# Kernel tuning notes

Measured on AMD Instinct MI355X. Metric: run time of the kernel, lower is better.

## Reference

```python
import jax, jax.numpy as jnp
import numpy as np

E, T, H, IN = 12, 2048, 64, 128  # edge types, notes, hidden, input feat


def setup_inputs() -> dict:
    key = jax.random.key(0)
    ks = jax.random.split(key, 9)
    std_a = (2.0 / (H + H)) ** 0.5
    std_b = (2.0 / (IN + H)) ** 0.5
    std_c = (2.0 / (H * E + H)) ** 0.5
    return {
        "input": jax.random.normal(ks[0], (1, T, IN), jnp.float32),
        "hidden": jax.random.normal(ks[1], (1, T, H), jnp.float32),
        # dense per-edge-type adjacency, scaled small for stable recurrence
        "edge_matrix": jax.random.normal(ks[2], (E, T, T), jnp.float32) * 0.05,
        "ba": jnp.zeros((E, H), jnp.float32),
        "wz_wr_wh": jax.random.normal(ks[3], (E, H, 3 * H), jnp.float32) * std_c,
        "uz_ur": jax.random.normal(ks[4], (H, 2 * H), jnp.float32) * std_a,
        "uh": jax.random.normal(ks[5], (H, H), jnp.float32) * std_a,
        "input_wzrh": jax.random.normal(ks[6], (IN, 3 * H), jnp.float32) * std_b,
        "bw": jnp.zeros((3 * H,), jnp.float32),
        "iteration": 10,
    }


def reference(input, hidden, edge_matrix, ba, wz_wr_wh, uz_ur, uh, input_wzrh, bw, iteration):
    x = input[0]   # [T, IN]  (batch == 1 in this branch)
    h0 = hidden[0]  # [T, H]
    # input projection is iteration-invariant; hoist it (same math as recompute)
    iwz, iwr, iwh = jnp.split(x @ input_wzrh, 3, axis=-1)  # each [T, H]

    def step(h, _):
        # activation[e,t,h] = sum_s edge[e,s,t] * hidden[s,h]  (transpose(1,2) bmm)
        act = jnp.einsum('est,sh->eth', edge_matrix, h) + ba[:, None, :]
        awzrh = jnp.einsum('eth,ehk->etk', act, wz_wr_wh) + bw  # [E, T, 3H]
        # split into z/r/h then sum over edge types (commutes with sum)
        awz, awr, awh = jnp.split(awzrh.sum(0), 3, axis=-1)      # each [T, H]
        awz = awz + iwz
        awr = awr + iwr
        awh = awh + iwh
        uz, ur = jnp.split(h @ uz_ur, 2, axis=-1)
        z = jax.nn.sigmoid(awz + uz)
        r = jax.nn.sigmoid(awr + ur)
        h_tilde = jnp.tanh(awh + (r * h) @ uh)
        return (1.0 - z) * h + z * h_tilde, None

    h, _ = jax.lax.scan(step, h0, None, length=iteration)
    return h[None]  # [1, T, H]
```

## Files before the change

kernel.cpp:

```cpp
#include <hip/hip_runtime.h>
#include <hip/hip_fp16.h>
#include <math.h>


constexpr int T   = 2048;
constexpr int H   = 64;
constexpr int E   = 12;
constexpr int FIN = 128;
constexpr int K3  = 192;
constexpr int ITER = 10;
constexpr int KSPLIT = 2;
constexpr int KSEG = T / KSPLIT;

#define SH   64.0f
#define SL   4096.0f
#define INV_HH (1.0f / 4096.0f)
#define INV_HL (1.0f / 16777216.0f)

typedef _Float16 half8 __attribute__((ext_vector_type(8)));
typedef float f32x4 __attribute__((ext_vector_type(4)));

__device__ __forceinline__ float sigmoidf_(float x) {
    return 1.0f / (1.0f + __expf(-x));
}
__device__ __forceinline__ void split16(float a, ushort& hi, ushort& lo) {
    float as = a * SH;
    __half h1 = __float2half(as);
    float r = (as - __half2float(h1)) * SL;
    __half h2 = __float2half(r);
    hi = __half_as_ushort(h1);
    lo = __half_as_ushort(h2);
}


__global__ __launch_bounds__(256) void const_kernel(const float* __restrict__ ba,
                                                    const float* __restrict__ W,
                                                    const float* __restrict__ bw,
                                                    float* __restrict__ constv) {
    __shared__ float red[256];
    const int k = blockIdx.x;
    const int tid = threadIdx.x;
    float s = 0.0f;
    for (int eh = tid; eh < E * H; eh += 256)
        s += ba[eh] * W[(size_t)eh * K3 + k];
    red[tid] = s;
    __syncthreads();
    for (int off = 128; off > 0; off >>= 1) {
        if (tid < off) red[tid] += red[tid + off];
        __syncthreads();
    }
    if (tid == 0) constv[k] = red[0] + (float)E * bw[k];
}

__global__ __launch_bounds__(256) void base_kernel(const float* __restrict__ x,
                                                   const float* __restrict__ iw,
                                                   const float* __restrict__ constv,
                                                   float* __restrict__ base) {
    int idx = blockIdx.x * 256 + threadIdx.x;
    int t = idx / K3, k = idx % K3;
    float acc = constv[k];
    const float* xr = x + (size_t)t * FIN;
    for (int j = 0; j < FIN; ++j)
        acc = fmaf(xr[j], iw[(size_t)j * K3 + k], acc);
    base[idx] = acc;
}

__global__ __launch_bounds__(256) void edgeT_kernel(const float* __restrict__ edge,
                                                    ushort* __restrict__ ehi,
                                                    ushort* __restrict__ elo) {
    __shared__ float til[64][65];
    const int t0 = blockIdx.x * 64;
    const int s0 = blockIdx.y * 64;
    const int e  = blockIdx.z;
    const int tid = threadIdx.x;
    const float* eb = edge + ((size_t)e * T + s0) * T + t0;
    #pragma unroll
    for (int p = 0; p < 4; ++p) {
        int idx = tid + p * 256;
        int r = idx >> 4, c4 = (idx & 15) << 2;
        float4 v = *reinterpret_cast<const float4*>(eb + (size_t)r * T + c4);
        til[r][c4] = v.x; til[r][c4 + 1] = v.y; til[r][c4 + 2] = v.z; til[r][c4 + 3] = v.w;
    }
    __syncthreads();
    #pragma unroll
    for (int p = 0; p < 2; ++p) {
        int q = tid + p * 256;
        int tt = q >> 3, cs = q & 7;
        ushort hb[8], lb[8];
        #pragma unroll
        for (int j = 0; j < 8; ++j)
            split16(til[cs * 8 + j][tt], hb[j], lb[j]);
        size_t off = ((size_t)e * T + t0 + tt) * T + s0 + cs * 8;
        *reinterpret_cast<uint4*>(ehi + off) = *reinterpret_cast<uint4*>(hb);
        *reinterpret_cast<uint4*>(elo + off) = *reinterpret_cast<uint4*>(lb);
    }
}

__global__ __launch_bounds__(256) void hsplit_kernel(const float* __restrict__ hbuf,
                                                     ushort* __restrict__ hhi,
                                                     ushort* __restrict__ hlo) {
    __shared__ float til[64][65];
    const int t0 = blockIdx.x * 64;
    const int tid = threadIdx.x;
    #pragma unroll
    for (int p = 0; p < 4; ++p) {
        int idx = tid + p * 256;
        int r = idx >> 4, c4 = (idx & 15) << 2;
        float4 v = *reinterpret_cast<const float4*>(hbuf + (size_t)(t0 + r) * H + c4);
        til[r][c4] = v.x; til[r][c4 + 1] = v.y; til[r][c4 + 2] = v.z; til[r][c4 + 3] = v.w;
    }
    __syncthreads();
    #pragma unroll
    for (int p = 0; p < 2; ++p) {
        int q = tid + p * 256;
        int hh = q >> 3, cs = q & 7;
        ushort hb[8], lb[8];
        #pragma unroll
        for (int j = 0; j < 8; ++j)
            split16(til[cs * 8 + j][hh], hb[j], lb[j]);
        size_t off = (size_t)hh * T + t0 + cs * 8;
        *reinterpret_cast<uint4*>(hhi + off) = *reinterpret_cast<uint4*>(hb);
        *reinterpret_cast<uint4*>(hlo + off) = *reinterpret_cast<uint4*>(lb);
    }
}

__global__ __launch_bounds__(256) void bmm_mfma_kernel(
        const ushort* __restrict__ Ahi, const ushort* __restrict__ Alo,
        const ushort* __restrict__ Bhi, const ushort* __restrict__ Blo,
        float* __restrict__ P2) {
    __shared__ ushort sAh[64 * 64], sAl[64 * 64], sBh[64 * 64], sBl[64 * 64];
    const int t0 = blockIdx.x * 64;
    const int e  = blockIdx.y;
    const int kz = blockIdx.z;
    const int tid  = threadIdx.x;
    const int lane = tid & 63;
    const int w    = tid >> 6;
    const int wm = w >> 1, wn = w & 1;

    const int r0 = tid >> 3;
    const int c0 = tid & 7;
    const int swz = (c0 ^ (r0 & 7)) << 4;
    const int o0 = r0 * 128 + swz;
    const int o1 = o0 + 32 * 128;

    const size_t ks0 = (size_t)kz * KSEG;
    const ushort* pA0 = Ahi + ((size_t)e * T + t0 + r0) * T + ks0 + c0 * 8;
    const ushort* pA1 = pA0 + (size_t)32 * T;
    const ushort* pL0 = Alo + ((size_t)e * T + t0 + r0) * T + ks0 + c0 * 8;
    const ushort* pL1 = pL0 + (size_t)32 * T;
    const ushort* pB0 = Bhi + (size_t)r0 * T + ks0 + c0 * 8;
    const ushort* pB1 = pB0 + (size_t)32 * T;
    const ushort* pC0 = Blo + (size_t)r0 * T + ks0 + c0 * 8;
    const ushort* pC1 = pC0 + (size_t)32 * T;

    char* bAh = (char*)sAh; char* bAl = (char*)sAl;
    char* bBh = (char*)sBh; char* bBl = (char*)sBl;

    f32x4 accH[2][2], accL[2][2];
    #pragma unroll
    for (int i = 0; i < 2; ++i)
        #pragma unroll
        for (int j = 0; j < 2; ++j) { accH[i][j] = (f32x4)(0.0f); accL[i][j] = (f32x4)(0.0f); }

    for (int kt = 0; kt < KSEG / 64; ++kt) {
        const int ko = kt * 64;
        uint4 va0 = *reinterpret_cast<const uint4*>(pA0 + ko);
        uint4 va1 = *reinterpret_cast<const uint4*>(pA1 + ko);
        uint4 vl0 = *reinterpret_cast<const uint4*>(pL0 + ko);
        uint4 vl1 = *reinterpret_cast<const uint4*>(pL1 + ko);
        uint4 vb0 = *reinterpret_cast<const uint4*>(pB0 + ko);
        uint4 vb1 = *reinterpret_cast<const uint4*>(pB1 + ko);
        uint4 vc0 = *reinterpret_cast<const uint4*>(pC0 + ko);
        uint4 vc1 = *reinterpret_cast<const uint4*>(pC1 + ko);
        __syncthreads();
        *reinterpret_cast<uint4*>(bAh + o0) = va0;
        *reinterpret_cast<uint4*>(bAh + o1) = va1;
        *reinterpret_cast<uint4*>(bAl + o0) = vl0;
        *reinterpret_cast<uint4*>(bAl + o1) = vl1;
        *reinterpret_cast<uint4*>(bBh + o0) = vb0;
        *reinterpret_cast<uint4*>(bBh + o1) = vb1;
        *reinterpret_cast<uint4*>(bBl + o0) = vc0;
        *reinterpret_cast<uint4*>(bBl + o1) = vc1;
        __syncthreads();

        half8 fah[2][2], fal[2][2], fbh[2][2], fbl[2][2];
        #pragma unroll
        for (int mi = 0; mi < 2; ++mi)
            #pragma unroll
            for (int kk = 0; kk < 2; ++kk) {
                int row = wm * 32 + mi * 16 + (lane & 15);
                int ch  = kk * 4 + (lane >> 4);
                int off = row * 128 + (((ch ^ (row & 7))) << 4);
                fah[mi][kk] = *reinterpret_cast<const half8*>(bAh + off);
                fal[mi][kk] = *reinterpret_cast<const half8*>(bAl + off);
            }
        #pragma unroll
        for (int ni = 0; ni < 2; ++ni)
            #pragma unroll
            for (int kk = 0; kk < 2; ++kk) {
                int row = wn * 32 + ni * 16 + (lane & 15);
                int ch  = kk * 4 + (lane >> 4);
                int off = row * 128 + (((ch ^ (row & 7))) << 4);
                fbh[ni][kk] = *reinterpret_cast<const half8*>(bBh + off);
                fbl[ni][kk] = *reinterpret_cast<const half8*>(bBl + off);
            }
        #pragma unroll
        for (int mi = 0; mi < 2; ++mi)
            #pragma unroll
            for (int ni = 0; ni < 2; ++ni)
                #pragma unroll
                for (int kk = 0; kk < 2; ++kk) {
                    accH[mi][ni] = __builtin_amdgcn_mfma_f32_16x16x32_f16(
                        fah[mi][kk], fbh[ni][kk], accH[mi][ni], 0, 0, 0);
                    accL[mi][ni] = __builtin_amdgcn_mfma_f32_16x16x32_f16(
                        fah[mi][kk], fbl[ni][kk], accL[mi][ni], 0, 0, 0);
                    accL[mi][ni] = __builtin_amdgcn_mfma_f32_16x16x32_f16(
                        fal[mi][kk], fbh[ni][kk], accL[mi][ni], 0, 0, 0);
                }
    }

    float* outp = P2 + (((size_t)kz * E + e) * T + t0) * H;
    #pragma unroll
    for (int mi = 0; mi < 2; ++mi)
        #pragma unroll
        for (int ni = 0; ni < 2; ++ni)
            #pragma unroll
            for (int j = 0; j < 4; ++j) {
                int row = wm * 32 + mi * 16 + (lane >> 4) * 4 + j;
                int col = wn * 32 + ni * 16 + (lane & 15);
                outp[(size_t)row * H + col] =
                    accH[mi][ni][j] * INV_HH + accL[mi][ni][j] * INV_HL;
            }
}

constexpr int BMM_BM = 64;
constexpr int BMM_BK = 32;
__global__ __launch_bounds__(128) void bmm_kernel(const float* __restrict__ edge,
                                                  const float* __restrict__ hbuf,
                                                  float* __restrict__ P) {
    __shared__ float As[BMM_BK][68];
    __shared__ float Bs[BMM_BK][68];
    const int e  = blockIdx.y;
    const int t0 = blockIdx.x * BMM_BM;
    const int tid = threadIdx.x;
    const int ty = tid >> 4;
    const int tx = tid & 15;
    const float* eb = edge + (size_t)e * T * T;
    float acc[8][4];
    #pragma unroll
    for (int i = 0; i < 8; ++i)
        #pragma unroll
        for (int j = 0; j < 4; ++j) acc[i][j] = 0.0f;
    for (int s0 = 0; s0 < T; s0 += BMM_BK) {
        #pragma unroll
        for (int p = 0; p < 4; ++p) {
            int idx = tid + p * 128;
            int r = idx >> 4, c4 = (idx & 15) << 2;
            *reinterpret_cast<float4*>(&As[r][c4]) =
                *reinterpret_cast<const float4*>(eb + (size_t)(s0 + r) * T + t0 + c4);
            *reinterpret_cast<float4*>(&Bs[r][c4]) =
                *reinterpret_cast<const float4*>(hbuf + (size_t)(s0 + r) * H + c4);
        }
        __syncthreads();
        #pragma unroll
        for (int k = 0; k < BMM_BK; ++k) {
            float a[8], b[4];
            *reinterpret_cast<float4*>(&a[0]) = *reinterpret_cast<const float4*>(&As[k][ty * 8]);
            *reinterpret_cast<float4*>(&a[4]) = *reinterpret_cast<const float4*>(&As[k][ty * 8 + 4]);
            *reinterpret_cast<float4*>(&b[0]) = *reinterpret_cast<const float4*>(&Bs[k][tx * 4]);
            #pragma unroll
            for (int i = 0; i < 8; ++i)
                #pragma unroll
                for (int j = 0; j < 4; ++j)
                    acc[i][j] = fmaf(a[i], b[j], acc[i][j]);
        }
        __syncthreads();
    }
    float* pb = P + ((size_t)e * T + t0) * H;
    #pragma unroll
    for (int i = 0; i < 8; ++i) {
        float4 v = make_float4(acc[i][0], acc[i][1], acc[i][2], acc[i][3]);
        *reinterpret_cast<float4*>(pb + (size_t)(ty * 8 + i) * H + tx * 4) = v;
    }
}

__global__ __launch_bounds__(256) void proj_kernel(const float* __restrict__ P2,
                                                   const float* __restrict__ W,
                                                   float* __restrict__ partial,
                                                   int ksplit) {
    __shared__ float Ps[64][68];
    __shared__ float Ws[H][K3];
    const int e  = blockIdx.y;
    const int t0 = blockIdx.x * 64;
    const int tid = threadIdx.x;
    const float* pb = P2 + ((size_t)e * T + t0) * H;
    const size_t SL2 = (size_t)E * T * H;
    const float* wb = W + (size_t)e * H * K3;
    #pragma unroll
    for (int p = 0; p < 4; ++p) {
        int idx = tid + p * 256;
        int r = idx >> 4, c4 = (idx & 15) << 2;
        float4 v = *reinterpret_cast<const float4*>(pb + (size_t)r * H + c4);
        if (ksplit == 2) {
            float4 u = *reinterpret_cast<const float4*>(pb + SL2 + (size_t)r * H + c4);
            v.x += u.x; v.y += u.y; v.z += u.z; v.w += u.w;
        }
        *reinterpret_cast<float4*>(&Ps[r][c4]) = v;
    }
    #pragma unroll
    for (int p = 0; p < 12; ++p) {
        int idx = tid + p * 256;
        int r = idx / 48, c4 = (idx % 48) << 2;
        *reinterpret_cast<float4*>(&Ws[r][c4]) =
            *reinterpret_cast<const float4*>(wb + (size_t)r * K3 + c4);
    }
    __syncthreads();
    const int ty = tid >> 4;
    const int tx = tid & 15;
    float acc[4][12];
    #pragma unroll
    for (int i = 0; i < 4; ++i)
        #pragma unroll
        for (int c = 0; c < 12; ++c) acc[i][c] = 0.0f;
    for (int h = 0; h < H; ++h) {
        float a[4], b[12];
        #pragma unroll
        for (int i = 0; i < 4; ++i) a[i] = Ps[ty * 4 + i][h];
        *reinterpret_cast<float4*>(&b[0]) = *reinterpret_cast<const float4*>(&Ws[h][tx * 12]);
        *reinterpret_cast<float4*>(&b[4]) = *reinterpret_cast<const float4*>(&Ws[h][tx * 12 + 4]);
        *reinterpret_cast<float4*>(&b[8]) = *reinterpret_cast<const float4*>(&Ws[h][tx * 12 + 8]);
        #pragma unroll
        for (int i = 0; i < 4; ++i)
            #pragma unroll
            for (int c = 0; c < 12; ++c)
                acc[i][c] = fmaf(a[i], b[c], acc[i][c]);
    }
    float* ob = partial + ((size_t)e * T + t0) * K3;
    #pragma unroll
    for (int i = 0; i < 4; ++i) {
        float* orow = ob + (size_t)(ty * 4 + i) * K3 + tx * 12;
        *reinterpret_cast<float4*>(orow)     = make_float4(acc[i][0], acc[i][1], acc[i][2],  acc[i][3]);
        *reinterpret_cast<float4*>(orow + 4) = make_float4(acc[i][4], acc[i][5], acc[i][6],  acc[i][7]);
        *reinterpret_cast<float4*>(orow + 8) = make_float4(acc[i][8], acc[i][9], acc[i][10], acc[i][11]);
    }
}

__global__ __launch_bounds__(256) void gru_kernel(float* __restrict__ hbuf,
                                                  const float* __restrict__ partial,
                                                  const float* __restrict__ base,
                                                  const float* __restrict__ uzur,
                                                  const float* __restrict__ uhm) {
    __shared__ float Uzr[H][2 * H];
    __shared__ float Uh[H][H];
    __shared__ float hrow[16][68];
    __shared__ float rh[16][68];
    const int t0 = blockIdx.x * 16;
    const int tid = threadIdx.x;
    #pragma unroll
    for (int p = 0; p < 8; ++p) {
        int idx = tid + p * 256;
        int r = idx >> 5, c4 = (idx & 31) << 2;
        *reinterpret_cast<float4*>(&Uzr[r][c4]) =
            *reinterpret_cast<const float4*>(uzur + (size_t)r * 2 * H + c4);
    }
    #pragma unroll
    for (int p = 0; p < 4; ++p) {
        int idx = tid + p * 256;
        int r = idx >> 4, c4 = (idx & 15) << 2;
        *reinterpret_cast<float4*>(&Uh[r][c4]) =
            *reinterpret_cast<const float4*>(uhm + (size_t)r * H + c4);
    }
    {
        int r = tid >> 4, c4 = (tid & 15) << 2;
        *reinterpret_cast<float4*>(&hrow[r][c4]) =
            *reinterpret_cast<const float4*>(hbuf + (size_t)(t0 + r) * H + c4);
    }
    __syncthreads();
    const int row = tid >> 4, cg = tid & 15;
    const int t = t0 + row, j0 = cg * 4;

    float az[4], ar[4], ah[4];
    const float* bp = base + (size_t)t * K3;
    {
        float4 b0 = *reinterpret_cast<const float4*>(bp + j0);
        float4 b1 = *reinterpret_cast<const float4*>(bp + 64 + j0);
        float4 b2 = *reinterpret_cast<const float4*>(bp + 128 + j0);
        az[0]=b0.x; az[1]=b0.y; az[2]=b0.z; az[3]=b0.w;
        ar[0]=b1.x; ar[1]=b1.y; ar[2]=b1.z; ar[3]=b1.w;
        ah[0]=b2.x; ah[1]=b2.y; ah[2]=b2.z; ah[3]=b2.w;
    }
    #pragma unroll
    for (int e = 0; e < E; ++e) {
        const float* pp = partial + ((size_t)e * T + t) * K3;
        float4 v0 = *reinterpret_cast<const float4*>(pp + j0);
        float4 v1 = *reinterpret_cast<const float4*>(pp + 64 + j0);
        float4 v2 = *reinterpret_cast<const float4*>(pp + 128 + j0);
        az[0]+=v0.x; az[1]+=v0.y; az[2]+=v0.z; az[3]+=v0.w;
        ar[0]+=v1.x; ar[1]+=v1.y; ar[2]+=v1.z; ar[3]+=v1.w;
        ah[0]+=v2.x; ah[1]+=v2.y; ah[2]+=v2.z; ah[3]+=v2.w;
    }
    float hv[4];
    #pragma unroll
    for (int c = 0; c < 4; ++c) hv[c] = hrow[row][j0 + c];

    float uz[4] = {0,0,0,0}, ur[4] = {0,0,0,0};
    for (int hh = 0; hh < H; ++hh) {
        float hs = hrow[row][hh];
        #pragma unroll
        for (int c = 0; c < 4; ++c) {
            uz[c] = fmaf(hs, Uzr[hh][j0 + c], uz[c]);
            ur[c] = fmaf(hs, Uzr[hh][64 + j0 + c], ur[c]);
        }
    }
    float z[4], rr[4];
    #pragma unroll
    for (int c = 0; c < 4; ++c) {
        z[c]  = sigmoidf_(az[c] + uz[c]);
        rr[c] = sigmoidf_(ar[c] + ur[c]);
        rh[row][j0 + c] = rr[c] * hv[c];
    }
    __syncthreads();
    float uht[4] = {0,0,0,0};
    for (int hh = 0; hh < H; ++hh) {
        float rs = rh[row][hh];
        #pragma unroll
        for (int c = 0; c < 4; ++c)
            uht[c] = fmaf(rs, Uh[hh][j0 + c], uht[c]);
    }
    float hn[4];
    #pragma unroll
    for (int c = 0; c < 4; ++c) {
        float ht = tanhf(ah[c] + uht[c]);
        hn[c] = (1.0f - z[c]) * hv[c] + z[c] * ht;
    }
    *reinterpret_cast<float4*>(hbuf + (size_t)t * H + j0) =
        make_float4(hn[0], hn[1], hn[2], hn[3]);
}

extern "C" void kernel_launch(void* const* d_in, const int* in_sizes, int n_in,
                              void* d_out, int out_size, void* d_ws, size_t ws_size,
                              hipStream_t stream) {
    const float* x    = (const float*)d_in[0];
    const float* h0   = (const float*)d_in[1];
    const float* edge = (const float*)d_in[2];
    const float* ba   = (const float*)d_in[3];
    const float* W    = (const float*)d_in[4];
    const float* uzur = (const float*)d_in[5];
    const float* uhm  = (const float*)d_in[6];
    const float* iw   = (const float*)d_in[7];
    const float* bw   = (const float*)d_in[8];
    float* out = (float*)d_out;

    float* ws = (float*)d_ws;
    float* hbuf    = ws;
    float* basep   = hbuf + (size_t)T * H;
    float* constv  = basep + (size_t)T * K3;
    float* P2      = constv + 256;
    float* partial = P2 + (size_t)KSPLIT * E * T * H;
    ushort* hT_hi  = (ushort*)(partial + (size_t)E * T * K3);
    ushort* hT_lo  = hT_hi + (size_t)H * T;
    ushort* eT_hi  = hT_lo + (size_t)H * T;
    ushort* eT_lo  = eT_hi + (size_t)E * T * T;

    const size_t NEED_MFMA =
        (size_t)((char*)(eT_lo + (size_t)E * T * T) - (char*)d_ws);
    const bool useMfma = ws_size >= NEED_MFMA;

    hipMemcpyAsync(hbuf, h0, sizeof(float) * T * H, hipMemcpyDeviceToDevice, stream);
    const_kernel<<<K3, 256, 0, stream>>>(ba, W, bw, constv);
    base_kernel<<<(T * K3) / 256, 256, 0, stream>>>(x, iw, constv, basep);

    if (useMfma) {
        edgeT_kernel<<<dim3(T / 64, T / 64, E), 256, 0, stream>>>(edge, eT_hi, eT_lo);
        for (int it = 0; it < ITER; ++it) {
            hsplit_kernel<<<T / 64, 256, 0, stream>>>(hbuf, hT_hi, hT_lo);
            bmm_mfma_kernel<<<dim3(T / 64, E, KSPLIT), 256, 0, stream>>>(
                eT_hi, eT_lo, hT_hi, hT_lo, P2);
            proj_kernel<<<dim3(T / 64, E), 256, 0, stream>>>(P2, W, partial, 2);
            gru_kernel<<<T / 16, 256, 0, stream>>>(hbuf, partial, basep, uzur, uhm);
        }
    } else {
        for (int it = 0; it < ITER; ++it) {
            bmm_kernel<<<dim3(T / BMM_BM, E), 128, 0, stream>>>(edge, hbuf, P2);
            proj_kernel<<<dim3(T / 64, E), 256, 0, stream>>>(P2, W, partial, 1);
            gru_kernel<<<T / 16, 256, 0, stream>>>(hbuf, partial, basep, uzur, uhm);
        }
    }
    hipMemcpyAsync(out, hbuf, sizeof(float) * T * H, hipMemcpyDeviceToDevice, stream);
}
```

Baseline: 1.232 ms.

## Pre-tile swizzled fp16 operands and double-buffer MFMA bmm via direct global-to-LDS loads

The edge and hidden split kernels now write operands in contiguous pre-swizzled 64x64 tiles, so the bmm kernel can copy whole tiles straight into LDS with global_load_lds and double buffering, overlapping the next tile's load with the current MFMA work. The K split goes from 2 to 4 to put more blocks in flight, and proj_kernel now sums a variable number of partial slices. The intent is to hide global memory latency and drop the register round trip on each load, at the cost of more partial-sum traffic, more LDS per block, and a layout that assumes T is a multiple of 64.

Result: no change. 1.251 ms (+1.5%).

```diff
diff --git a/kernel.cpp b/kernel.cpp
--- a/kernel.cpp
+++ b/kernel.cpp
@@ -9,8 +9,10 @@
 constexpr int FIN = 128;
 constexpr int K3  = 192;
 constexpr int ITER = 10;
-constexpr int KSPLIT = 2;
+constexpr int KSPLIT = 4;
 constexpr int KSEG = T / KSPLIT;
+constexpr int NT_PER_KZ = KSEG / 64;
+constexpr int TILE_US = 4096;
 
 #define SH   64.0f
 #define SL   4096.0f
@@ -19,6 +21,13 @@
 
 typedef _Float16 half8 __attribute__((ext_vector_type(8)));
 typedef float f32x4 __attribute__((ext_vector_type(4)));
+
+typedef const __attribute__((address_space(1))) unsigned int* gas_uint_ptr;
+typedef __attribute__((address_space(3))) unsigned int* las_uint_ptr;
+
+__device__ __forceinline__ void gload_lds16(const void* g, void* l) {
+    __builtin_amdgcn_global_load_lds((gas_uint_ptr)g, (las_uint_ptr)l, 16, 0, 0);
+}
 
 __device__ __forceinline__ float sigmoidf_(float x) {
     return 1.0f / (1.0f + __expf(-x));
@@ -82,17 +91,18 @@
         til[r][c4] = v.x; til[r][c4 + 1] = v.y; til[r][c4 + 2] = v.z; til[r][c4 + 3] = v.w;
     }
     __syncthreads();
+    size_t tbase = ((size_t)(e * 32 + blockIdx.x) * 32 + blockIdx.y) * TILE_US;
     #pragma unroll
     for (int p = 0; p < 2; ++p) {
         int q = tid + p * 256;
-        int tt = q >> 3, cs = q & 7;
+        int tt = q >> 3, c = q & 7;
+        int lc = c ^ (tt & 7);
         ushort hb[8], lb[8];
         #pragma unroll
         for (int j = 0; j < 8; ++j)
-            split16(til[cs * 8 + j][tt], hb[j], lb[j]);
-        size_t off = ((size_t)e * T + t0 + tt) * T + s0 + cs * 8;
-        *reinterpret_cast<uint4*>(ehi + off) = *reinterpret_cast<uint4*>(hb);
-        *reinterpret_cast<uint4*>(elo + off) = *reinterpret_cast<uint4*>(lb);
+            split16(til[lc * 8 + j][tt], hb[j], lb[j]);
+        *reinterpret_cast<uint4*>(ehi + tbase + q * 8) = *reinterpret_cast<uint4*>(hb);
+        *reinterpret_cast<uint4*>(elo + tbase + q * 8) = *reinterpret_cast<uint4*>(lb);
     }
 }
 
@@ -110,17 +120,18 @@
         til[r][c4] = v.x; til[r][c4 + 1] = v.y; til[r][c4 + 2] = v.z; til[r][c4 + 3] = v.w;
     }
     __syncthreads();
+    size_t tbase = (size_t)blockIdx.x * TILE_US;
     #pragma unroll
     for (int p = 0; p < 2; ++p) {
         int q = tid + p * 256;
-        int hh = q >> 3, cs = q & 7;
+        int hh = q >> 3, c = q & 7;
+        int lc = c ^ (hh & 7);
         ushort hb[8], lb[8];
         #pragma unroll
         for (int j = 0; j < 8; ++j)
-            split16(til[cs * 8 + j][hh], hb[j], lb[j]);
-        size_t off = (size_t)hh * T + t0 + cs * 8;
-        *reinterpret_cast<uint4*>(hhi + off) = *reinterpret_cast<uint4*>(hb);
-        *reinterpret_cast<uint4*>(hlo + off) = *reinterpret_cast<uint4*>(lb);
+            split16(til[lc * 8 + j][hh], hb[j], lb[j]);
+        *reinterpret_cast<uint4*>(hhi + tbase + q * 8) = *reinterpret_cast<uint4*>(hb);
+        *reinterpret_cast<uint4*>(hlo + tbase + q * 8) = *reinterpret_cast<uint4*>(lb);
     }
 }
 
@@ -128,8 +139,8 @@
         const ushort* __restrict__ Ahi, const ushort* __restrict__ Alo,
         const ushort* __restrict__ Bhi, const ushort* __restrict__ Blo,
         float* __restrict__ P2) {
-    __shared__ ushort sAh[64 * 64], sAl[64 * 64], sBh[64 * 64], sBl[64 * 64];
-    const int t0 = blockIdx.x * 64;
+    __shared__ __align__(1024) char smem[2][4][8192];
+    const int tb = blockIdx.x;
     const int e  = blockIdx.y;
     const int kz = blockIdx.z;
     const int tid  = threadIdx.x;
@@ -137,24 +148,23 @@
     const int w    = tid >> 6;
     const int wm = w >> 1, wn = w & 1;
 
-    const int r0 = tid >> 3;
-    const int c0 = tid & 7;
-    const int swz = (c0 ^ (r0 & 7)) << 4;
-    const int o0 = r0 * 128 + swz;
-    const int o1 = o0 + 32 * 128;
-
-    const size_t ks0 = (size_t)kz * KSEG;
-    const ushort* pA0 = Ahi + ((size_t)e * T + t0 + r0) * T + ks0 + c0 * 8;
-    const ushort* pA1 = pA0 + (size_t)32 * T;
-    const ushort* pL0 = Alo + ((size_t)e * T + t0 + r0) * T + ks0 + c0 * 8;
-    const ushort* pL1 = pL0 + (size_t)32 * T;
-    const ushort* pB0 = Bhi + (size_t)r0 * T + ks0 + c0 * 8;
-    const ushort* pB1 = pB0 + (size_t)32 * T;
-    const ushort* pC0 = Blo + (size_t)r0 * T + ks0 + c0 * 8;
-    const ushort* pC1 = pC0 + (size_t)32 * T;
-
-    char* bAh = (char*)sAh; char* bAl = (char*)sAl;
-    char* bBh = (char*)sBh; char* bBl = (char*)sBl;
+    const char* gsrc[4];
+    gsrc[0] = (const char*)(Ahi + ((size_t)(e * 32 + tb) * 32 + kz * NT_PER_KZ) * TILE_US);
+    gsrc[1] = (const char*)(Alo + ((size_t)(e * 32 + tb) * 32 + kz * NT_PER_KZ) * TILE_US);
+    gsrc[2] = (const char*)(Bhi + (size_t)(kz * NT_PER_KZ) * TILE_US);
+    gsrc[3] = (const char*)(Blo + (size_t)(kz * NT_PER_KZ) * TILE_US);
+
+    int offA[2][2], offB[2][2];
+    #pragma unroll
+    for (int mi = 0; mi < 2; ++mi)
+        #pragma unroll
+        for (int u = 0; u < 2; ++u) {
+            int rowA = wm * 32 + mi * 16 + (lane & 15);
+            int rowB = wn * 32 + mi * 16 + (lane & 15);
+            int kc = u * 4 + (lane >> 4);
+            offA[mi][u] = rowA * 128 + ((kc ^ (rowA & 7)) << 4);
+            offB[mi][u] = rowB * 128 + ((kc ^ (rowB & 7)) << 4);
+        }
 
     f32x4 accH[2][2], accL[2][2];
     #pragma unroll
@@ -162,63 +172,59 @@
         #pragma unroll
         for (int j = 0; j < 2; ++j) { accH[i][j] = (f32x4)(0.0f); accL[i][j] = (f32x4)(0.0f); }
 
-    for (int kt = 0; kt < KSEG / 64; ++kt) {
-        const int ko = kt * 64;
-        uint4 va0 = *reinterpret_cast<const uint4*>(pA0 + ko);
-        uint4 va1 = *reinterpret_cast<const uint4*>(pA1 + ko);
-        uint4 vl0 = *reinterpret_cast<const uint4*>(pL0 + ko);
-        uint4 vl1 = *reinterpret_cast<const uint4*>(pL1 + ko);
-        uint4 vb0 = *reinterpret_cast<const uint4*>(pB0 + ko);
-        uint4 vb1 = *reinterpret_cast<const uint4*>(pB1 + ko);
-        uint4 vc0 = *reinterpret_cast<const uint4*>(pC0 + ko);
-        uint4 vc1 = *reinterpret_cast<const uint4*>(pC1 + ko);
+    auto stage_all = [&](int b, int kt) {
+        #pragma unroll
+        for (int m = 0; m < 4; ++m) {
+            const char* g = gsrc[m] + (size_t)kt * 8192;
+            #pragma unroll
+            for (int p = 0; p < 2; ++p) {
+                int q = tid + p * 256;
+                gload_lds16(g + q * 16, &smem[b][m][(q >> 6) << 10]);
+            }
+        }
+    };
+
+    auto compute = [&](int b) {
+        const char* bAh = smem[b][0];
+        const char* bAl = smem[b][1];
+        const char* bBh = smem[b][2];
+        const char* bBl = smem[b][3];
+        half8 fah[2][2], fal[2][2], fbh[2][2], fbl[2][2];
+        #pragma unroll
+        for (int mi = 0; mi < 2; ++mi)
+            #pragma unroll
+            for (int u = 0; u < 2; ++u) {
+                fah[mi][u] = *reinterpret_cast<const half8*>(bAh + offA[mi][u]);
+                fal[mi][u] = *reinterpret_cast<const half8*>(bAl + offA[mi][u]);
+                fbh[mi][u] = *reinterpret_cast<const half8*>(bBh + offB[mi][u]);
+                fbl[mi][u] = *reinterpret_cast<const half8*>(bBl + offB[mi][u]);
+            }
+        #pragma unroll
+        for (int u = 0; u < 2; ++u)
+            #pragma unroll
+            for (int mi = 0; mi < 2; ++mi)
+                #pragma unroll
+                for (int ni = 0; ni < 2; ++ni) {
+                    accH[mi][ni] = __builtin_amdgcn_mfma_f32_16x16x32_f16(
+                        fah[mi][u], fbh[ni][u], accH[mi][ni], 0, 0, 0);
+                    accL[mi][ni] = __builtin_amdgcn_mfma_f32_16x16x32_f16(
+                        fah[mi][u], fbl[ni][u], accL[mi][ni], 0, 0, 0);
+                    accL[mi][ni] = __builtin_amdgcn_mfma_f32_16x16x32_f16(
+                        fal[mi][u], fbh[ni][u], accL[mi][ni], 0, 0, 0);
+                }
+    };
+
+    int cur = 0;
+    stage_all(0, 0);
+    __syncthreads();
+    for (int kt = 0; kt < NT_PER_KZ; ++kt) {
+        if (kt < NT_PER_KZ - 1) stage_all(cur ^ 1, kt + 1);
+        compute(cur);
         __syncthreads();
-        *reinterpret_cast<uint4*>(bAh + o0) = va0;
-        *reinterpret_cast<uint4*>(bAh + o1) = va1;
-        *reinterpret_cast<uint4*>(bAl + o0) = vl0;
-        *reinterpret_cast<uint4*>(bAl + o1) = vl1;
-        *reinterpret_cast<uint4*>(bBh + o0) = vb0;
-        *reinterpret_cast<uint4*>(bBh + o1) = vb1;
-        *reinterpret_cast<uint4*>(bBl + o0) = vc0;
-        *reinterpret_cast<uint4*>(bBl + o1) = vc1;
-        __syncthreads();
-
-        half8 fah[2][2], fal[2][2], fbh[2][2], fbl[2][2];
-        #pragma unroll
-        for (int mi = 0; mi < 2; ++mi)
-            #pragma unroll
-            for (int kk = 0; kk < 2; ++kk) {
-                int row = wm * 32 + mi * 16 + (lane & 15);
-                int ch  = kk * 4 + (lane >> 4);
-                int off = row * 128 + (((ch ^ (row & 7))) << 4);
-                fah[mi][kk] = *reinterpret_cast<const half8*>(bAh + off);
-                fal[mi][kk] = *reinterpret_cast<const half8*>(bAl + off);
-            }
-        #pragma unroll
-        for (int ni = 0; ni < 2; ++ni)
-            #pragma unroll
-            for (int kk = 0; kk < 2; ++kk) {
-                int row = wn * 32 + ni * 16 + (lane & 15);
-                int ch  = kk * 4 + (lane >> 4);
-                int off = row * 128 + (((ch ^ (row & 7))) << 4);
-                fbh[ni][kk] = *reinterpret_cast<const half8*>(bBh + off);
-                fbl[ni][kk] = *reinterpret_cast<const half8*>(bBl + off);
-            }
-        #pragma unroll
-        for (int mi = 0; mi < 2; ++mi)
-            #pragma unroll
-            for (int ni = 0; ni < 2; ++ni)
-                #pragma unroll
-                for (int kk = 0; kk < 2; ++kk) {
-                    accH[mi][ni] = __builtin_amdgcn_mfma_f32_16x16x32_f16(
-                        fah[mi][kk], fbh[ni][kk], accH[mi][ni], 0, 0, 0);
-                    accL[mi][ni] = __builtin_amdgcn_mfma_f32_16x16x32_f16(
-                        fah[mi][kk], fbl[ni][kk], accL[mi][ni], 0, 0, 0);
-                    accL[mi][ni] = __builtin_amdgcn_mfma_f32_16x16x32_f16(
-                        fal[mi][kk], fbh[ni][kk], accL[mi][ni], 0, 0, 0);
-                }
-    }
-
+        cur ^= 1;
+    }
+
+    const int t0 = tb * 64;
     float* outp = P2 + (((size_t)kz * E + e) * T + t0) * H;
     #pragma unroll
     for (int mi = 0; mi < 2; ++mi)
@@ -301,8 +307,8 @@
         int idx = tid + p * 256;
         int r = idx >> 4, c4 = (idx & 15) << 2;
         float4 v = *reinterpret_cast<const float4*>(pb + (size_t)r * H + c4);
-        if (ksplit == 2) {
-            float4 u = *reinterpret_cast<const float4*>(pb + SL2 + (size_t)r * H + c4);
+        for (int z = 1; z < ksplit; ++z) {
+            float4 u = *reinterpret_cast<const float4*>(pb + (size_t)z * SL2 + (size_t)r * H + c4);
             v.x += u.x; v.y += u.y; v.z += u.z; v.w += u.w;
         }
         *reinterpret_cast<float4*>(&Ps[r][c4]) = v;
@@ -471,18 +477,18 @@
     base_kernel<<<(T * K3) / 256, 256, 0, stream>>>(x, iw, constv, basep);
 
     if (useMfma) {
-        edgeT_kernel<<<dim3(T / 64, T / 64, E), 256, 0, stream>>>(edge, eT_hi, eT_lo);
+        edgeT_kernel<<<dim3(32, 32, E), 256, 0, stream>>>(edge, eT_hi, eT_lo);
         for (int it = 0; it < ITER; ++it) {
-            hsplit_kernel<<<T / 64, 256, 0, stream>>>(hbuf, hT_hi, hT_lo);
-            bmm_mfma_kernel<<<dim3(T / 64, E, KSPLIT), 256, 0, stream>>>(
+            hsplit_kernel<<<32, 256, 0, stream>>>(hbuf, hT_hi, hT_lo);
+            bmm_mfma_kernel<<<dim3(32, E, KSPLIT), 256, 0, stream>>>(
                 eT_hi, eT_lo, hT_hi, hT_lo, P2);
-            proj_kernel<<<dim3(T / 64, E), 256, 0, stream>>>(P2, W, partial, 2);
+            proj_kernel<<<dim3(32, E), 256, 0, stream>>>(P2, W, partial, KSPLIT);
             gru_kernel<<<T / 16, 256, 0, stream>>>(hbuf, partial, basep, uzur, uhm);
         }
     } else {
         for (int it = 0; it < ITER; ++it) {
             bmm_kernel<<<dim3(T / BMM_BM, E), 128, 0, stream>>>(edge, hbuf, P2);
-            proj_kernel<<<dim3(T / 64, E), 256, 0, stream>>>(P2, W, partial, 1);
+            proj_kernel<<<dim3(32, E), 256, 0, stream>>>(P2, W, partial, 1);
             gru_kernel<<<T / 16, 256, 0, stream>>>(hbuf, partial, basep, uzur, uhm);
         }
     }
```
